# Performance work log

Measured on AMD Instinct MI355X. Metric: run time of the kernel, lower is better.

## Reference

```python
import jax, jax.numpy as jnp
import numpy as np

N = 8192
F_IN = 256
F_OUT = 128
NEG = -9.0e15

def setup_inputs() -> dict:
    key = jax.random.key(0)
    k1, k2, k3, k4 = jax.random.split(key, 4)
    x = jax.random.normal(k1, (N, F_IN), dtype=jnp.float32)
    adj = jax.random.randint(k2, (N, N), 0, 2, dtype=jnp.int32)
    # xavier-uniform-ish scales
    W = jax.random.normal(k3, (F_IN, F_OUT), dtype=jnp.float32) * (1.414 / np.sqrt(F_IN))
    a = jax.random.normal(k4, (2 * F_OUT, 1), dtype=jnp.float32) * (1.414 / np.sqrt(F_OUT))
    return {"x": x, "adj": adj, "W": W, "a": a}

def reference(x, adj, W, a):
    # h_i = W^T x_i  -> [N, F_OUT]
    h = x @ W
    # torch builds atom_trans[i,j] = concat(h_i, h_j); e[i,j] = leakyrelu(a1.h_i + a2.h_j)
    a1 = a[:F_OUT, 0]   # [F_OUT]
    a2 = a[F_OUT:, 0]   # [F_OUT]
    s1 = h @ a1         # [N]
    s2 = h @ a2         # [N]
    e = jax.nn.leaky_relu(s1[:, None] + s2[None, :], negative_slope=0.01)  # [N, N]
    masked = jnp.where(adj > 0, e, jnp.full_like(e, NEG))
    attention = jax.nn.softmax(masked, axis=1)
    # dropout is identity in eval mode
    h1 = attention @ h  # [N, F_OUT]
    return jax.nn.elu(h1)
```

## Files before the change

### kernel.cpp

```cpp
#include <hip/hip_runtime.h>
#include <hip/hip_bf16.h>
#include <cstdint>
#include <cstddef>

#define NN 8192
#define FIN 256
#define FO 128
#define SPLITK 8
#define JCH 1024
#define NSB 8

typedef float f32x4 __attribute__((ext_vector_type(4)));
typedef _Float16 f16x8 __attribute__((ext_vector_type(8)));

typedef __attribute__((address_space(3))) void lds_void;
typedef const __attribute__((address_space(1))) void glb_void;
__device__ __forceinline__ void gl_lds16(const void* g, void* l) {
  __builtin_amdgcn_global_load_lds((glb_void*)g, (lds_void*)l, 16, 0, 0);
}

__device__ __forceinline__ unsigned enc_f32(float f) {
  unsigned u = __float_as_uint(f);
  return (u & 0x80000000u) ? ~u : (u | 0x80000000u);
}
__device__ __forceinline__ float dec_f32(unsigned u) {
  unsigned b = (u & 0x80000000u) ? (u ^ 0x80000000u) : ~u;
  return __uint_as_float(b);
}

__global__ void k1_xw(const float* __restrict__ x, const float* __restrict__ W,
                      float* __restrict__ h, unsigned* __restrict__ enc) {
  __shared__ float xs[32 * 66];
  __shared__ float Ws[64 * 128];
  int t = threadIdx.x;
  int r0 = blockIdx.x * 32;
  if (blockIdx.x == 0 && t == 0) *enc = 0u;
  int r = t & 31, cg = t >> 5;
  float acc[16];
#pragma unroll
  for (int i = 0; i < 16; ++i) acc[i] = 0.f;
  for (int ko = 0; ko < 4; ++ko) {
    __syncthreads();
    {
      int rr = t >> 3, kc = (t & 7) * 8;
      const float2* src = (const float2*)(x + (size_t)(r0 + rr) * FIN + ko * 64 + kc);
      float2* dst = (float2*)&xs[rr * 66 + kc];
#pragma unroll
      for (int q = 0; q < 4; ++q) dst[q] = src[q];
    }
    {
      int kk = t >> 2, q = t & 3;
      const float4* src = (const float4*)(W + (size_t)(ko * 64 + kk) * FO + q * 32);
      float4* dst = (float4*)&Ws[kk * 128 + q * 32];
#pragma unroll
      for (int i = 0; i < 8; ++i) dst[i] = src[i];
    }
    __syncthreads();
#pragma unroll 8
    for (int kk = 0; kk < 64; ++kk) {
      float xv = xs[r * 66 + kk];
      const float4* wr = (const float4*)&Ws[kk * 128 + cg * 16];
      float4 w0 = wr[0], w1 = wr[1], w2 = wr[2], w3 = wr[3];
      acc[0]  = fmaf(xv, w0.x, acc[0]);  acc[1]  = fmaf(xv, w0.y, acc[1]);
      acc[2]  = fmaf(xv, w0.z, acc[2]);  acc[3]  = fmaf(xv, w0.w, acc[3]);
      acc[4]  = fmaf(xv, w1.x, acc[4]);  acc[5]  = fmaf(xv, w1.y, acc[5]);
      acc[6]  = fmaf(xv, w1.z, acc[6]);  acc[7]  = fmaf(xv, w1.w, acc[7]);
      acc[8]  = fmaf(xv, w2.x, acc[8]);  acc[9]  = fmaf(xv, w2.y, acc[9]);
      acc[10] = fmaf(xv, w2.z, acc[10]); acc[11] = fmaf(xv, w2.w, acc[11]);
      acc[12] = fmaf(xv, w3.x, acc[12]); acc[13] = fmaf(xv, w3.y, acc[13]);
      acc[14] = fmaf(xv, w3.z, acc[14]); acc[15] = fmaf(xv, w3.w, acc[15]);
    }
  }
  float* hp = h + (size_t)(r0 + r) * FO + cg * 16;
#pragma unroll
  for (int i = 0; i < 4; ++i)
    ((float4*)hp)[i] = make_float4(acc[4 * i], acc[4 * i + 1], acc[4 * i + 2], acc[4 * i + 3]);
}

__global__ void k2_prep(const float* __restrict__ h, const float* __restrict__ a,
                        _Float16* __restrict__ hT,
                        float* __restrict__ s1, float* __restrict__ s2,
                        unsigned* __restrict__ enc) {
  __shared__ float ht[64 * 129];
  int t = threadIdx.x;
  int r0 = blockIdx.x * 64;
  {
    int rr = t >> 2, q = t & 3;
    const float4* src = (const float4*)(h + (size_t)(r0 + rr) * FO + q * 32);
    float* dst = &ht[rr * 129 + q * 32];
#pragma unroll
    for (int i = 0; i < 8; ++i) {
      float4 v = src[i];
      dst[4 * i + 0] = v.x; dst[4 * i + 1] = v.y;
      dst[4 * i + 2] = v.z; dst[4 * i + 3] = v.w;
    }
  }
  __syncthreads();
  {
    int c = t >> 1, half = t & 1;
    alignas(16) _Float16 buf[32];
#pragma unroll
    for (int i = 0; i < 32; ++i) buf[i] = (_Float16)ht[(half * 32 + i) * 129 + c];
    int4* d = (int4*)(hT + (size_t)c * NN + r0 + half * 32);
#pragma unroll
    for (int i = 0; i < 4; ++i) d[i] = ((const int4*)buf)[i];
  }
  if (t < 64) {
    int row = r0 + t;
    float v1 = 0.f, v2 = 0.f;
#pragma unroll 16
    for (int c = 0; c < FO; ++c) {
      float hv = ht[t * 129 + c];
      v1 = fmaf(hv, a[c], v1);
      v2 = fmaf(hv, a[FO + c], v2);
    }
    s1[row] = v1; s2[row] = v2;
    float m = v2;
#pragma unroll
    for (int off = 1; off < 64; off <<= 1) m = fmaxf(m, __shfl_xor(m, off));
    if (t == 0) atomicMax(enc, enc_f32(m));
  }
}

__device__ __forceinline__ _Float16 wel(unsigned av, float s2v, float s1v, float mv, float& sum) {
  float tt = s1v + s2v;
  tt = fmaxf(tt, 0.01f * tt);
  float wf = av ? __expf(tt - mv) : 0.f;
  _Float16 wh = (_Float16)wf;
  sum += (float)wh;
  return wh;
}

#define K4COMPUTE(MEV, MOD, BUFI, SBASE)                                         \
  {                                                                              \
    _Pragma("unroll")                                                            \
    for (int ks = 0; ks < 2; ++ks) {                                             \
      unsigned ne = ((MEV) >> (ks * 16 + kgrp * 4)) & 0xfu;                      \
      unsigned no = ((MOD) >> (ks * 16 + kgrp * 4)) & 0xfu;                      \
      int jloc = (SBASE) + ks * 32 + kgrp * 8;                                   \
      f32x4 sa = *(const f32x4*)&s2l[jloc];                                      \
      f32x4 sb = *(const f32x4*)&s2l[jloc + 4];                                  \
      f16x8 af;                                                                  \
      af[0] = wel(ne & 1u, sa[0], s10, m0, sum0);                                \
      af[1] = wel(no & 1u, sa[1], s10, m0, sum0);                                \
      af[2] = wel(ne & 2u, sa[2], s10, m0, sum0);                                \
      af[3] = wel(no & 2u, sa[3], s10, m0, sum0);                                \
      af[4] = wel(ne & 4u, sb[0], s10, m0, sum0);                                \
      af[5] = wel(no & 4u, sb[1], s10, m0, sum0);                                \
      af[6] = wel(ne & 8u, sb[2], s10, m0, sum0);                                \
      af[7] = wel(no & 8u, sb[3], s10, m0, sum0);                                \
      _Pragma("unroll")                                                          \
      for (int cf = 0; cf < 8; ++cf) {                                           \
        f16x8 bfr = *(const f16x8*)&tile[BUFI][(cf * 16 + l15) * 64 +            \
                       ((ks * 32 + kgrp * 8) ^ (l7 * 8))];                       \
        acc[cf] = __builtin_amdgcn_mfma_f32_16x16x32_f16(af, bfr, acc[cf], 0, 0, 0); \
      }                                                                          \
    }                                                                            \
  }

__global__ void __launch_bounds__(256, 4) k4_main(
    const int* __restrict__ adj, const float* __restrict__ s1g,
    const float* __restrict__ s2g, const unsigned* __restrict__ enc,
    const _Float16* __restrict__ hT,
    float* __restrict__ num_p, float* __restrict__ den_p) {
  __shared__ _Float16 tile[2][128 * 64];
  __shared__ float s2l[JCH];
  int t = threadIdx.x;
  int l = t & 63, wv = t >> 6;
  int l15 = l & 15, kgrp = l >> 4;
  int l7 = l15 & 7;
  int split = blockIdx.x;
  int r0 = blockIdx.y * 64;
  int jbeg = split * JCH;
  int row = r0 + wv * 16 + l15;

  float c2 = dec_f32(*enc);
  float s10 = s1g[row];
  float m0 = s10 + c2; m0 = fmaxf(m0, 0.01f * m0);

  f32x4 acc[8];
#pragma unroll
  for (int cf = 0; cf < 8; ++cf) acc[cf] = (f32x4){0.f, 0.f, 0.f, 0.f};
  float sum0 = 0.f;
  const int* abase = adj + (size_t)(r0 + wv * 16) * NN + 2 * l;

  auto stage = [&](int b, int jg) {
    const _Float16* g0 = hT + (size_t)(wv * 32 + (l >> 3)) * NN + jg +
                         (((l & 7) ^ (l >> 3)) * 8);
    _Float16* base = &tile[b][(wv * 32) * 64];
    gl_lds16(g0, base);
    gl_lds16(g0 + (size_t)8 * NN, base + 8 * 64);
    gl_lds16(g0 + (size_t)16 * NN, base + 16 * 64);
    gl_lds16(g0 + (size_t)24 * NN, base + 24 * 64);
  };

  int2 S[16];
#define LOADSET2(J)                                                              \
  _Pragma("unroll")                                                              \
  for (int rr = 0; rr < 16; ++rr)                                                \
    S[rr] = *(const int2*)(abase + (size_t)rr * NN + (J));

  unsigned mev_lo, mev_hi, mod_lo, mod_hi;
#define BALLOTROUTE()                                                            \
  {                                                                              \
    mev_lo = 0u; mev_hi = 0u; mod_lo = 0u; mod_hi = 0u;                          \
    _Pragma("unroll")                                                            \
    for (int rr = 0; rr < 16; ++rr) {                                            \
      unsigned long long be = __ballot(S[rr].x > 0);                             \
      unsigned long long bo = __ballot(S[rr].y > 0);                             \
      bool sel = (l15 == rr);                                                    \
      mev_lo = sel ? (unsigned)be : mev_lo;                                      \
      mev_hi = sel ? (unsigned)(be >> 32) : mev_hi;                              \
      mod_lo = sel ? (unsigned)bo : mod_lo;                                      \
      mod_hi = sel ? (unsigned)(bo >> 32) : mod_hi;                              \
    }                                                                            \
  }

  stage(0, jbeg);
  LOADSET2(jbeg)
  *(float4*)&s2l[t * 4] = *(const float4*)(s2g + jbeg + t * 4);
  asm volatile("s_waitcnt vmcnt(0) lgkmcnt(0)" ::: "memory");
  __builtin_amdgcn_s_barrier();
  __builtin_amdgcn_sched_barrier(0);
  BALLOTROUTE()

#pragma unroll 1
  for (int sb = 0; sb < NSB; ++sb) {
    int sjb = jbeg + sb * 128;
    int sbase = sb * 128;
    stage(1, sjb + 64);
    if (sb + 1 < NSB) { LOADSET2(sjb + 128) }
    __builtin_amdgcn_sched_barrier(0);
    K4COMPUTE(mev_lo, mod_lo, 0, sbase)
    __builtin_amdgcn_sched_barrier(0);
    if (sb + 1 < NSB) asm volatile("s_waitcnt vmcnt(16)" ::: "memory");
    else              asm volatile("s_waitcnt vmcnt(0)" ::: "memory");
    __builtin_amdgcn_s_barrier();
    __builtin_amdgcn_sched_barrier(0);
    if (sb + 1 < NSB) stage(0, sjb + 128);
    __builtin_amdgcn_sched_barrier(0);
    K4COMPUTE(mev_hi, mod_hi, 1, sbase + 64)
    __builtin_amdgcn_sched_barrier(0);
    if (sb + 1 < NSB) {
      asm volatile("s_waitcnt vmcnt(0)" ::: "memory");
      __builtin_amdgcn_s_barrier();
      __builtin_amdgcn_sched_barrier(0);
      BALLOTROUTE()
    }
  }

  sum0 += __shfl_xor(sum0, 16);
  sum0 += __shfl_xor(sum0, 32);
  size_t sbase2 = (size_t)split * NN;
  if (l < 16) den_p[sbase2 + r0 + wv * 16 + l] = sum0;
#pragma unroll
  for (int cf = 0; cf < 8; ++cf) {
#pragma unroll
    for (int i = 0; i < 4; ++i) {
      int orow = r0 + wv * 16 + kgrp * 4 + i;
      int ocol = cf * 16 + l15;
      num_p[(sbase2 + orow) * (size_t)FO + ocol] = acc[cf][i];
    }
  }
}

__global__ void k5_fin(const float* __restrict__ num_p, const float* __restrict__ den_p,
                       float* __restrict__ out) {
  int idx = blockIdx.x * 256 + threadIdx.x;
  int row = idx >> 7;
  float num = 0.f, den = 0.f;
#pragma unroll
  for (int s = 0; s < SPLITK; ++s) {
    num += num_p[(size_t)s * (NN * FO) + idx];
    den += den_p[(size_t)s * NN + row];
  }
  float v = num / den;
  out[idx] = v > 0.f ? v : expm1f(v);
}

extern "C" void kernel_launch(void* const* d_in, const int* in_sizes, int n_in,
                              void* d_out, int out_size, void* d_ws, size_t ws_size,
                              hipStream_t stream) {
  const float* x   = (const float*)d_in[0];
  const int*   adj = (const int*)d_in[1];
  const float* W   = (const float*)d_in[2];
  const float* a   = (const float*)d_in[3];
  float* out = (float*)d_out;
  char* ws = (char*)d_ws;

  float*     h     = (float*)ws;
  _Float16*  hT    = (_Float16*)(ws + ((size_t)4 << 20));
  float*     s1    = (float*)(ws + ((size_t)6 << 20));
  float*     s2    = (float*)(ws + ((size_t)6 << 20) + (32u << 10));
  unsigned*  enc   = (unsigned*)(ws + ((size_t)6 << 20) + (64u << 10));
  float*     den_p = (float*)(ws + ((size_t)6 << 20) + (128u << 10));
  float*     num_p = (float*)(ws + ((size_t)7 << 20));

  k1_xw<<<dim3(256), dim3(256), 0, stream>>>(x, W, h, enc);
  k2_prep<<<dim3(128), dim3(256), 0, stream>>>(h, a, hT, s1, s2, enc);
  k4_main<<<dim3(SPLITK, 128), dim3(256), 0, stream>>>(adj, s1, s2, enc, hT,
                                                       num_p, den_p);
  k5_fin<<<dim3((NN * FO) / 256), dim3(256), 0, stream>>>(num_p, den_p, out);
}
```

Before: 120.2 us.

## Process two 16-row groups per wave with triple-buffered hT tiles

Each wave now handles 32 rows (two MFMA accumulator sets) that share every B-fragment read from LDS, doubling reuse of the staged hT tile. This halves the grid to 64 row-blocks. hT staging moves to a three-deep LDS ring, and adjacency loads become int4 with a 4-way ballot routing, pipelined across 256-column spans. The cost is higher register pressure (launch bounds lowered to 2 blocks/CU), more LDS, and fewer blocks in flight.

```diff
diff --git a/kernel.cpp b/kernel.cpp
--- a/kernel.cpp
+++ b/kernel.cpp
@@ -8,10 +8,11 @@
 #define FO 128
 #define SPLITK 8
 #define JCH 1024
-#define NSB 8
+#define TILE_E (128 * 64)
 
 typedef float f32x4 __attribute__((ext_vector_type(4)));
 typedef _Float16 f16x8 __attribute__((ext_vector_type(8)));
+typedef unsigned long long ull;
 
 typedef __attribute__((address_space(3))) void lds_void;
 typedef const __attribute__((address_space(1))) void glb_void;
@@ -131,58 +132,103 @@
   return wh;
 }
 
-#define K4COMPUTE(MEV, MOD, BUFI, SBASE)                                         \
+#define LOADSET4(BASE, J)                                                        \
+  _Pragma("unroll")                                                              \
+  for (int rr = 0; rr < 16; ++rr)                                                \
+    S[rr] = *(const int4*)((BASE) + (size_t)rr * NN + (J) + 4 * l);
+
+#define ROUTE4(W0, W1, W2, W3)                                                   \
   {                                                                              \
+    ull a0 = 0, a1 = 0, a2 = 0, a3 = 0;                                          \
+    _Pragma("unroll")                                                            \
+    for (int rr = 0; rr < 16; ++rr) {                                            \
+      ull bx = __ballot(S[rr].x > 0);                                            \
+      ull by = __ballot(S[rr].y > 0);                                            \
+      ull bz = __ballot(S[rr].z > 0);                                            \
+      ull bw = __ballot(S[rr].w > 0);                                            \
+      bool sel = (l15 == rr);                                                    \
+      a0 = sel ? bx : a0; a1 = sel ? by : a1;                                    \
+      a2 = sel ? bz : a2; a3 = sel ? bw : a3;                                    \
+    }                                                                            \
+    W0 = a0 >> sh2; W1 = a1 >> sh2; W2 = a2 >> sh2; W3 = a3 >> sh2;              \
+  }
+
+#define AFRAG(AF, W0, W1, W2, W3, SH, SA4, SB4, S1V, MV, SUM)                    \
+  {                                                                              \
+    unsigned b0 = (unsigned)((W0) >> (SH));                                      \
+    unsigned b1 = (unsigned)((W1) >> (SH));                                      \
+    unsigned b2 = (unsigned)((W2) >> (SH));                                      \
+    unsigned b3 = (unsigned)((W3) >> (SH));                                      \
+    AF[0] = wel(b0 & 1u, SA4[0], S1V, MV, SUM);                                  \
+    AF[1] = wel(b1 & 1u, SA4[1], S1V, MV, SUM);                                  \
+    AF[2] = wel(b2 & 1u, SA4[2], S1V, MV, SUM);                                  \
+    AF[3] = wel(b3 & 1u, SA4[3], S1V, MV, SUM);                                  \
+    AF[4] = wel(b0 & 2u, SB4[0], S1V, MV, SUM);                                  \
+    AF[5] = wel(b1 & 2u, SB4[1], S1V, MV, SUM);                                  \
+    AF[6] = wel(b2 & 2u, SB4[2], S1V, MV, SUM);                                  \
+    AF[7] = wel(b3 & 2u, SB4[3], S1V, MV, SUM);                                  \
+  }
+
+#define BODYCOMP(P, T)                                                           \
+  {                                                                              \
+    const _Float16* tb = tbase + ((T) % 3) * TILE_E;                             \
     _Pragma("unroll")                                                            \
     for (int ks = 0; ks < 2; ++ks) {                                             \
-      unsigned ne = ((MEV) >> (ks * 16 + kgrp * 4)) & 0xfu;                      \
-      unsigned no = ((MOD) >> (ks * 16 + kgrp * 4)) & 0xfu;                      \
-      int jloc = (SBASE) + ks * 32 + kgrp * 8;                                   \
+      int jloc = (T) * 64 + ks * 32 + kgrp * 8;                                  \
       f32x4 sa = *(const f32x4*)&s2l[jloc];                                      \
       f32x4 sb = *(const f32x4*)&s2l[jloc + 4];                                  \
-      f16x8 af;                                                                  \
-      af[0] = wel(ne & 1u, sa[0], s10, m0, sum0);                                \
-      af[1] = wel(no & 1u, sa[1], s10, m0, sum0);                                \
-      af[2] = wel(ne & 2u, sa[2], s10, m0, sum0);                                \
-      af[3] = wel(no & 2u, sa[3], s10, m0, sum0);                                \
-      af[4] = wel(ne & 4u, sb[0], s10, m0, sum0);                                \
-      af[5] = wel(no & 4u, sb[1], s10, m0, sum0);                                \
-      af[6] = wel(ne & 8u, sb[2], s10, m0, sum0);                                \
-      af[7] = wel(no & 8u, sb[3], s10, m0, sum0);                                \
+      f16x8 afA, afB;                                                            \
+      AFRAG(afA, mA0, mA1, mA2, mA3, (P) * 16 + ks * 8, sa, sb, s1A, mvA, sumA)  \
+      AFRAG(afB, mBc0, mBc1, mBc2, mBc3, (P) * 16 + ks * 8, sa, sb, s1B, mvB, sumB) \
       _Pragma("unroll")                                                          \
       for (int cf = 0; cf < 8; ++cf) {                                           \
-        f16x8 bfr = *(const f16x8*)&tile[BUFI][(cf * 16 + l15) * 64 +            \
+        f16x8 bfr = *(const f16x8*)&tb[(cf * 16 + l15) * 64 +                    \
                        ((ks * 32 + kgrp * 8) ^ (l7 * 8))];                       \
-        acc[cf] = __builtin_amdgcn_mfma_f32_16x16x32_f16(af, bfr, acc[cf], 0, 0, 0); \
+        accA[cf] = __builtin_amdgcn_mfma_f32_16x16x32_f16(afA, bfr, accA[cf], 0, 0, 0); \
+        accB[cf] = __builtin_amdgcn_mfma_f32_16x16x32_f16(afB, bfr, accB[cf], 0, 0, 0); \
       }                                                                          \
     }                                                                            \
   }
 
-__global__ void __launch_bounds__(256, 4) k4_main(
+#define ENDBODY(VM)                                                              \
+  __builtin_amdgcn_sched_barrier(0);                                             \
+  asm volatile("s_waitcnt vmcnt(" #VM ")" ::: "memory");                         \
+  __builtin_amdgcn_s_barrier();                                                  \
+  __builtin_amdgcn_sched_barrier(0);
+
+__global__ void __launch_bounds__(256, 2) k4_main(
     const int* __restrict__ adj, const float* __restrict__ s1g,
     const float* __restrict__ s2g, const unsigned* __restrict__ enc,
     const _Float16* __restrict__ hT,
     float* __restrict__ num_p, float* __restrict__ den_p) {
-  __shared__ _Float16 tile[2][128 * 64];
+  __shared__ _Float16 tile[3][TILE_E];
   __shared__ float s2l[JCH];
   int t = threadIdx.x;
   int l = t & 63, wv = t >> 6;
   int l15 = l & 15, kgrp = l >> 4;
   int l7 = l15 & 7;
+  int sh2 = kgrp * 2;
   int split = blockIdx.x;
-  int r0 = blockIdx.y * 64;
+  int r0 = blockIdx.y * 128;
   int jbeg = split * JCH;
-  int row = r0 + wv * 16 + l15;
-
+
+  int rowA = r0 + wv * 32 + l15;
+  int rowB = rowA + 16;
   float c2 = dec_f32(*enc);
-  float s10 = s1g[row];
-  float m0 = s10 + c2; m0 = fmaxf(m0, 0.01f * m0);
-
-  f32x4 acc[8];
-#pragma unroll
-  for (int cf = 0; cf < 8; ++cf) acc[cf] = (f32x4){0.f, 0.f, 0.f, 0.f};
-  float sum0 = 0.f;
-  const int* abase = adj + (size_t)(r0 + wv * 16) * NN + 2 * l;
+  float s1A = s1g[rowA], s1B = s1g[rowB];
+  float mvA = s1A + c2; mvA = fmaxf(mvA, 0.01f * mvA);
+  float mvB = s1B + c2; mvB = fmaxf(mvB, 0.01f * mvB);
+
+  f32x4 accA[8], accB[8];
+#pragma unroll
+  for (int cf = 0; cf < 8; ++cf) {
+    accA[cf] = (f32x4){0.f, 0.f, 0.f, 0.f};
+    accB[cf] = (f32x4){0.f, 0.f, 0.f, 0.f};
+  }
+  float sumA = 0.f, sumB = 0.f;
+  const int* aA = adj + (size_t)(r0 + wv * 32) * NN;
+  const int* aB = aA + (size_t)16 * NN;
+  const _Float16* tbase = &tile[0][0];
 
   auto stage = [&](int b, int jg) {
     const _Float16* g0 = hT + (size_t)(wv * 32 + (l >> 3)) * NN + jg +
@@ -194,72 +240,76 @@
     gl_lds16(g0 + (size_t)24 * NN, base + 24 * 64);
   };
 
-  int2 S[16];
-#define LOADSET2(J)                                                              \
-  _Pragma("unroll")                                                              \
-  for (int rr = 0; rr < 16; ++rr)                                                \
-    S[rr] = *(const int2*)(abase + (size_t)rr * NN + (J));
-
-  unsigned mev_lo, mev_hi, mod_lo, mod_hi;
-#define BALLOTROUTE()                                                            \
-  {                                                                              \
-    mev_lo = 0u; mev_hi = 0u; mod_lo = 0u; mod_hi = 0u;                          \
-    _Pragma("unroll")                                                            \
-    for (int rr = 0; rr < 16; ++rr) {                                            \
-      unsigned long long be = __ballot(S[rr].x > 0);                             \
-      unsigned long long bo = __ballot(S[rr].y > 0);                             \
-      bool sel = (l15 == rr);                                                    \
-      mev_lo = sel ? (unsigned)be : mev_lo;                                      \
-      mev_hi = sel ? (unsigned)(be >> 32) : mev_hi;                              \
-      mod_lo = sel ? (unsigned)bo : mod_lo;                                      \
-      mod_hi = sel ? (unsigned)(bo >> 32) : mod_hi;                              \
-    }                                                                            \
-  }
+  int4 S[16];
+  ull mA0, mA1, mA2, mA3;
+  ull mBc0, mBc1, mBc2, mBc3;
+  ull mBn0, mBn1, mBn2, mBn3;
 
   stage(0, jbeg);
-  LOADSET2(jbeg)
+  stage(1, jbeg + 64);
+  LOADSET4(aA, jbeg)
+  ROUTE4(mA0, mA1, mA2, mA3)
+  LOADSET4(aB, jbeg)
   *(float4*)&s2l[t * 4] = *(const float4*)(s2g + jbeg + t * 4);
+  ROUTE4(mBc0, mBc1, mBc2, mBc3)
   asm volatile("s_waitcnt vmcnt(0) lgkmcnt(0)" ::: "memory");
   __builtin_amdgcn_s_barrier();
   __builtin_amdgcn_sched_barrier(0);
-  BALLOTROUTE()
 
 #pragma unroll 1
-  for (int sb = 0; sb < NSB; ++sb) {
-    int sjb = jbeg + sb * 128;
-    int sbase = sb * 128;
-    stage(1, sjb + 64);
-    if (sb + 1 < NSB) { LOADSET2(sjb + 128) }
+  for (int k = 0; k < 3; ++k) {
+    int t0 = 4 * k;
+    stage((t0 + 2) % 3, jbeg + (t0 + 2) * 64);
+    if (k) { ROUTE4(mA0, mA1, mA2, mA3) }
+    LOADSET4(aB, jbeg + (k + 1) * 256)
+    if (k) { mBc0 = mBn0; mBc1 = mBn1; mBc2 = mBn2; mBc3 = mBn3; }
     __builtin_amdgcn_sched_barrier(0);
-    K4COMPUTE(mev_lo, mod_lo, 0, sbase)
+    BODYCOMP(0, t0)
+    ENDBODY(20)
+    stage((t0 + 3) % 3, jbeg + (t0 + 3) * 64);
     __builtin_amdgcn_sched_barrier(0);
-    if (sb + 1 < NSB) asm volatile("s_waitcnt vmcnt(16)" ::: "memory");
-    else              asm volatile("s_waitcnt vmcnt(0)" ::: "memory");
-    __builtin_amdgcn_s_barrier();
+    BODYCOMP(1, t0 + 1)
+    ENDBODY(20)
+    stage((t0 + 4) % 3, jbeg + (t0 + 4) * 64);
+    ROUTE4(mBn0, mBn1, mBn2, mBn3)
+    LOADSET4(aA, jbeg + (k + 1) * 256)
     __builtin_amdgcn_sched_barrier(0);
-    if (sb + 1 < NSB) stage(0, sjb + 128);
+    BODYCOMP(2, t0 + 2)
+    ENDBODY(20)
+    stage((t0 + 5) % 3, jbeg + (t0 + 5) * 64);
     __builtin_amdgcn_sched_barrier(0);
-    K4COMPUTE(mev_hi, mod_hi, 1, sbase + 64)
-    __builtin_amdgcn_sched_barrier(0);
-    if (sb + 1 < NSB) {
-      asm volatile("s_waitcnt vmcnt(0)" ::: "memory");
-      __builtin_amdgcn_s_barrier();
-      __builtin_amdgcn_sched_barrier(0);
-      BALLOTROUTE()
-    }
-  }
-
-  sum0 += __shfl_xor(sum0, 16);
-  sum0 += __shfl_xor(sum0, 32);
-  size_t sbase2 = (size_t)split * NN;
-  if (l < 16) den_p[sbase2 + r0 + wv * 16 + l] = sum0;
+    BODYCOMP(3, t0 + 3)
+    ENDBODY(20)
+  }
+  stage(14 % 3, jbeg + 14 * 64);
+  ROUTE4(mA0, mA1, mA2, mA3)
+  mBc0 = mBn0; mBc1 = mBn1; mBc2 = mBn2; mBc3 = mBn3;
+  __builtin_amdgcn_sched_barrier(0);
+  BODYCOMP(0, 12)
+  ENDBODY(4)
+  stage(15 % 3, jbeg + 15 * 64);
+  __builtin_amdgcn_sched_barrier(0);
+  BODYCOMP(1, 13)
+  ENDBODY(4)
+  BODYCOMP(2, 14)
+  ENDBODY(0)
+  BODYCOMP(3, 15)
+
+  sumA += __shfl_xor(sumA, 16); sumA += __shfl_xor(sumA, 32);
+  sumB += __shfl_xor(sumB, 16); sumB += __shfl_xor(sumB, 32);
+  size_t sb2 = (size_t)split * NN;
+  if (l < 16) {
+    den_p[sb2 + r0 + wv * 32 + l] = sumA;
+    den_p[sb2 + r0 + wv * 32 + 16 + l] = sumB;
+  }
 #pragma unroll
   for (int cf = 0; cf < 8; ++cf) {
 #pragma unroll
     for (int i = 0; i < 4; ++i) {
-      int orow = r0 + wv * 16 + kgrp * 4 + i;
+      int orow = r0 + wv * 32 + kgrp * 4 + i;
       int ocol = cf * 16 + l15;
-      num_p[(sbase2 + orow) * (size_t)FO + ocol] = acc[cf][i];
+      num_p[(sb2 + orow) * (size_t)FO + ocol] = accA[cf][i];
+      num_p[(sb2 + orow + 16) * (size_t)FO + ocol] = accB[cf][i];
     }
   }
 }
@@ -298,7 +348,7 @@
 
   k1_xw<<<dim3(256), dim3(256), 0, stream>>>(x, W, h, enc);
   k2_prep<<<dim3(128), dim3(256), 0, stream>>>(h, a, hT, s1, s2, enc);
-  k4_main<<<dim3(SPLITK, 128), dim3(256), 0, stream>>>(adj, s1, s2, enc, hT,
-                                                       num_p, den_p);
+  k4_main<<<dim3(SPLITK, 64), dim3(256), 0, stream>>>(adj, s1, s2, enc, hT,
+                                                      num_p, den_p);
   k5_fin<<<dim3((NN * FO) / 256), dim3(256), 0, stream>>>(num_p, den_p, out);
 }
```

Result: no change. 118.0 us (-1.8%).
